# Kernel tuning notes

Hardware: AMD Instinct MI355X
Metric: run time of the kernel (lower is better)

## Reference

```python
import jax, jax.numpy as jnp
import numpy as np

N_NODES = 50000
N_EDGES = 640000
IN_CH, HID_CH, OUT_CH = 128, 128, 64


def setup_inputs() -> dict:
    key = jax.random.key(0)
    k1, k2, k3, k4, k5, k6 = jax.random.split(key, 6)
    x = jax.random.normal(k1, (N_NODES, IN_CH), dtype=jnp.float32)
    edge_index = jax.random.randint(k2, (2, N_EDGES), 0, N_NODES, dtype=jnp.int64)
    # Glorot-style init for GCN weights, zero bias (PyG defaults)
    W1 = jax.random.normal(k3, (IN_CH, HID_CH), dtype=jnp.float32) * (1.0 / np.sqrt(IN_CH))
    b1 = jnp.zeros((HID_CH,), dtype=jnp.float32)
    W2 = jax.random.normal(k4, (HID_CH, OUT_CH), dtype=jnp.float32) * (1.0 / np.sqrt(HID_CH))
    b2 = jnp.zeros((OUT_CH,), dtype=jnp.float32)
    return {"x": x, "edge_index": edge_index, "W1": W1, "b1": b1, "W2": W2, "b2": b2}


def gcn_conv(x, edge_index, W, b):
    """PyG GCNConv: add self-loops, symmetric deg^-1/2 normalization, linear, scatter-add."""
    N = x.shape[0]
    h = x @ W  # [N, C_out]
    loop = jnp.arange(N, dtype=edge_index.dtype)
    row = jnp.concatenate([edge_index[0], loop])  # source nodes
    col = jnp.concatenate([edge_index[1], loop])  # destination nodes
    deg = jax.ops.segment_sum(jnp.ones_like(col, dtype=h.dtype), col, num_segments=N)
    deg_inv_sqrt = jnp.where(deg > 0, deg ** -0.5, 0.0)
    norm = deg_inv_sqrt[row] * deg_inv_sqrt[col]  # [E+N]
    msg = h[row] * norm[:, None]  # gather + scale
    out = jax.ops.segment_sum(msg, col, num_segments=N)  # scatter-add
    return out + b


def reference(x, edge_index, W1, b1, W2, b2):
    h = jax.nn.relu(gcn_conv(x, edge_index, W1, b1))
    return gcn_conv(h, edge_index, W2, b2)
```

## Files before the change

### kernel.cpp

```cpp
#include <hip/hip_runtime.h>

#define NN 50000
#define NE 640000
#define NBK 196
#define CHUNK 2560

typedef __attribute__((ext_vector_type(8))) short s8v;
typedef __attribute__((ext_vector_type(4))) float f4v;

__device__ __forceinline__ unsigned short f2bf(float x) {
  unsigned int u = __float_as_uint(x);
  return (unsigned short)((u + 0x7fffu + ((u >> 16) & 1u)) >> 16);
}
__device__ __forceinline__ float bfval(unsigned short h) {
  return __uint_as_float((unsigned int)h << 16);
}
__device__ __forceinline__ float2 bfpair(unsigned int u) {
  float2 r;
  r.x = __uint_as_float((u & 0xffffu) << 16);
  r.y = __uint_as_float(u & 0xffff0000u);
  return r;
}

__device__ __forceinline__ void gload_lds16(const void* g, void* l) {
  __builtin_amdgcn_global_load_lds(
      (const __attribute__((address_space(1))) void*)g,
      (__attribute__((address_space(3))) void*)l, 16, 0, 0);
}


__global__ __launch_bounds__(256) void wprep_kernel(
    const float* __restrict__ W1, const float* __restrict__ W2,
    unsigned short* __restrict__ wt1h, unsigned short* __restrict__ wt1l,
    unsigned short* __restrict__ wt2h, unsigned short* __restrict__ wt2l,
    int* __restrict__ bcnt, unsigned int* __restrict__ htz, unsigned int* __restrict__ z1z) {
  const int b = blockIdx.x;
  const int t = threadIdx.x;
  if (b == 96) {
    for (int i = t; i < 2 * NBK; i += 256) bcnt[i] = 0;
    if (t < 64) htz[t] = 0u;
    if (t < 64) z1z[t] = 0u;
    return;
  }
  int idx = b * 256 + t;
  if (idx < 16384) {
    int c = idx >> 7, k = idx & 127;
    float w = W1[k * 128 + c];
    unsigned short h = f2bf(w);
    wt1h[idx] = h;
    wt1l[idx] = f2bf(w - bfval(h));
  } else if (idx < 24576) {
    int i2 = idx - 16384;
    int c = i2 >> 7, k = i2 & 127;
    float w = W2[k * 64 + c];
    unsigned short h = f2bf(w);
    wt2h[i2] = h;
    wt2l[i2] = f2bf(w - bfval(h));
  }
}


__global__ __launch_bounds__(256) void bucket_count_kernel(const int* __restrict__ col,
                                                           int* __restrict__ bcnt) {
  __shared__ int h[NBK];
  const int tid = threadIdx.x;
  for (int i = tid; i < NBK; i += 256) h[i] = 0;
  __syncthreads();
  const int base = blockIdx.x * CHUNK;
  for (int i = tid; i < CHUNK; i += 256) atomicAdd(&h[col[base + i] >> 8], 1);
  __syncthreads();
  for (int i = tid; i < NBK; i += 256)
    if (h[i]) atomicAdd(&bcnt[i], h[i]);
}

__global__ __launch_bounds__(256) void bucket_scatter_kernel(
    const int* __restrict__ row, const int* __restrict__ col,
    const int* __restrict__ bcnt, int* __restrict__ bfill,
    unsigned int* __restrict__ ebuf) {
  __shared__ int h[NBK], gst[NBK], h2[NBK], boffl[NBK], sc[256];
  const int tid = threadIdx.x;
  for (int i = tid; i < NBK; i += 256) { h[i] = 0; h2[i] = 0; }
  int v = (tid < NBK) ? bcnt[tid] : 0;
  sc[tid] = v;
  __syncthreads();
  for (int off = 1; off < 256; off <<= 1) {
    int u = (tid >= off) ? sc[tid - off] : 0;
    __syncthreads();
    sc[tid] += u;
    __syncthreads();
  }
  if (tid < NBK) boffl[tid] = sc[tid] - v;
  __syncthreads();

  const int base = blockIdx.x * CHUNK;
  for (int i = tid; i < CHUNK; i += 256) atomicAdd(&h[col[base + i] >> 8], 1);
  __syncthreads();
  for (int i = tid; i < NBK; i += 256) gst[i] = h[i] ? atomicAdd(&bfill[i], h[i]) : 0;
  __syncthreads();
  for (int i = tid; i < CHUNK; i += 256) {
    int c = col[base + i];
    int b = c >> 8;
    int r = atomicAdd(&h2[b], 1);
    unsigned int packed = ((unsigned int)row[base + i] << 8) | (unsigned int)(c & 255);
    ebuf[boffl[b] + gst[b] + r] = packed;
  }
}

__global__ __launch_bounds__(256) void bucket_build_kernel(
    const unsigned int* __restrict__ ebuf, const int* __restrict__ bcnt,
    int* __restrict__ row_ptr, float* __restrict__ dis, int* __restrict__ csr, int n) {
  __shared__ int cnt[256], c2[256], lbase[256], wsum[4], sc[256], cb[256];
  const int tid = threadIdx.x;
  const int b = blockIdx.x;

  int v = (tid < NBK) ? bcnt[tid] : 0;
  sc[tid] = v;
  cb[tid] = v;
  cnt[tid] = 0;
  c2[tid] = 0;
  __syncthreads();
  for (int off = 1; off < 256; off <<= 1) {
    int u = (tid >= off) ? sc[tid - off] : 0;
    __syncthreads();
    sc[tid] += u;
    __syncthreads();
  }
  const int s1 = sc[b];
  const int s0 = s1 - cb[b];

  for (int i = s0 + tid; i < s1; i += 256) atomicAdd(&cnt[ebuf[i] & 255], 1);
  __syncthreads();

  const int lane = tid & 63, w = tid >> 6;
  int c = cnt[tid];
  int inc = c;
#pragma unroll
  for (int off = 1; off < 64; off <<= 1) {
    int u = __shfl_up(inc, off);
    if (lane >= off) inc += u;
  }
  if (lane == 63) wsum[w] = inc;
  __syncthreads();
  int wo = 0;
  for (int i = 0; i < w; ++i) wo += wsum[i];
  const int excl = wo + inc - c;

  const int node = b * 256 + tid;
  if (node <= n) row_ptr[node] = s0 + excl;
  if (node < n) dis[node] = rsqrtf((float)(c + 1));
  lbase[tid] = s0 + excl;
  __syncthreads();

  for (int i = s0 + tid; i < s1; i += 256) {
    unsigned int p = ebuf[i];
    int dl = p & 255;
    int r = atomicAdd(&c2[dl], 1);
    csr[lbase[dl] + r] = (int)(p >> 8);
  }
}


template <int BM, int NCOLS, bool AF32, bool OUTBF16>
__global__ __launch_bounds__(256) void gemm_mfma_kernel(
    const void* __restrict__ Av, const unsigned short* __restrict__ Bth,
    const unsigned short* __restrict__ Btl, const float* __restrict__ dis,
    void* __restrict__ outv, int M) {
  constexpr int WCOL = NCOLS / 64;
  constexpr int WROW = 4 / WCOL;
  constexpr int RG = BM / (WROW * 16);
  constexpr int A_BYTES = BM * 32 * (AF32 ? 4 : 2);
  constexpr int B_BYTES = NCOLS * 32 * 2;
  constexpr int TILE_BYTES = A_BYTES + 2 * B_BYTES;
  constexpr int STAGE_BYTES = 2 * TILE_BYTES;
  constexpr int EPI_PITCH = OUTBF16 ? (NCOLS + 8) : (NCOLS + 4);
  constexpr int EPI_BYTES = BM * EPI_PITCH * (OUTBF16 ? 2 : 4);
  constexpr int SMEM_BYTES = STAGE_BYTES > EPI_BYTES ? STAGE_BYTES : EPI_BYTES;

  __shared__ __align__(16) unsigned char smem[SMEM_BYTES];

  const int t = threadIdx.x;
  const int lane = t & 63;
  const int l15 = lane & 15;
  const int lg = lane >> 4;
  const int wv = t >> 6;
  const int wr = wv % WROW;
  const int wc = wv / WROW;
  const int rb = blockIdx.x * BM;

  auto stage = [&](int kt, int buf) {
    unsigned char* base = smem + buf * TILE_BYTES;
    if constexpr (AF32) {
      constexpr int CPW = (BM * 128 / 1024) / 4;
#pragma unroll
      for (int j = 0; j < CPW; ++j) {
        int callr = (wv * CPW + j) * 8;
        int gr = min(rb + callr + (lane >> 3), M - 1);
        const float* gp = (const float*)Av + (size_t)gr * 128 + kt * 32 + (lane & 7) * 4;
        gload_lds16(gp, base + callr * 128);
      }
    } else {
      constexpr int CPW = (BM * 64 / 1024) / 4;
#pragma unroll
      for (int j = 0; j < CPW; ++j) {
        int callr = (wv * CPW + j) * 16;
        int gr = min(rb + callr + (lane >> 2), M - 1);
        const unsigned short* gp =
            (const unsigned short*)Av + (size_t)gr * 128 + kt * 32 + (lane & 3) * 8;
        gload_lds16(gp, base + callr * 64);
      }
    }
    {
      constexpr int CPW = (NCOLS * 64 / 1024) / 4;
#pragma unroll
      for (int j = 0; j < CPW; ++j) {
        int callr = (wv * CPW + j) * 16;
        int r = callr + (lane >> 2);
        size_t goff = (size_t)r * 128 + kt * 32 + (lane & 3) * 8;
        gload_lds16(Bth + goff, base + A_BYTES + callr * 64);
        gload_lds16(Btl + goff, base + A_BYTES + B_BYTES + callr * 64);
      }
    }
  };

  f4v acc[RG][4];
#pragma unroll
  for (int i = 0; i < RG; ++i)
#pragma unroll
    for (int j = 0; j < 4; ++j) acc[i][j] = (f4v){0.f, 0.f, 0.f, 0.f};

  stage(0, 0);
  __syncthreads();

#pragma unroll
  for (int kt = 0; kt < 4; ++kt) {
    const int buf = kt & 1;
    if (kt < 3) stage(kt + 1, buf ^ 1);

    const unsigned char* tb = smem + buf * TILE_BYTES;
    s8v afh[RG], afl[RG];
#pragma unroll
    for (int rg = 0; rg < RG; ++rg) {
      int row = wr * (RG * 16) + rg * 16 + l15;
      if constexpr (AF32) {
        const float* ap = (const float*)tb + row * 32 + lg * 8;
        float4 x0 = *reinterpret_cast<const float4*>(ap);
        float4 x1 = *reinterpret_cast<const float4*>(ap + 4);
        float f[8] = {x0.x, x0.y, x0.z, x0.w, x1.x, x1.y, x1.z, x1.w};
#pragma unroll
        for (int q = 0; q < 8; ++q) {
          unsigned short hq = f2bf(f[q]);
          afh[rg][q] = (short)hq;
          afl[rg][q] = (short)f2bf(f[q] - bfval(hq));
        }
      } else {
        afh[rg] = *reinterpret_cast<const s8v*>((const unsigned short*)tb + row * 32 + lg * 8);
      }
    }
#pragma unroll
    for (int cg = 0; cg < 4; ++cg) {
      int colr = wc * 64 + cg * 16 + l15;
      s8v bh = *reinterpret_cast<const s8v*>(
          (const unsigned short*)(tb + A_BYTES) + colr * 32 + lg * 8);
      s8v bl = *reinterpret_cast<const s8v*>(
          (const unsigned short*)(tb + A_BYTES + B_BYTES) + colr * 32 + lg * 8);
#pragma unroll
      for (int rg = 0; rg < RG; ++rg) {
        acc[rg][cg] = __builtin_amdgcn_mfma_f32_16x16x32_bf16(afh[rg], bh, acc[rg][cg], 0, 0, 0);
        acc[rg][cg] = __builtin_amdgcn_mfma_f32_16x16x32_bf16(afh[rg], bl, acc[rg][cg], 0, 0, 0);
        if constexpr (AF32)
          acc[rg][cg] = __builtin_amdgcn_mfma_f32_16x16x32_bf16(afl[rg], bh, acc[rg][cg], 0, 0, 0);
      }
    }
    __syncthreads();
  }

  float dv[RG][4];
#pragma unroll
  for (int rg = 0; rg < RG; ++rg)
#pragma unroll
    for (int g = 0; g < 4; ++g) {
      int r = rb + wr * (RG * 16) + rg * 16 + lg * 4 + g;
      dv[rg][g] = (r < M) ? dis[r] : 0.f;
    }

#pragma unroll
  for (int rg = 0; rg < RG; ++rg)
#pragma unroll
    for (int cg = 0; cg < 4; ++cg) {
      int colc = wc * 64 + cg * 16 + l15;
#pragma unroll
      for (int g = 0; g < 4; ++g) {
        int r = wr * (RG * 16) + rg * 16 + lg * 4 + g;
        float o = acc[rg][cg][g] * dv[rg][g];
        if constexpr (OUTBF16)
          ((unsigned short*)smem)[r * EPI_PITCH + colc] = f2bf(o);
        else
          ((float*)smem)[r * EPI_PITCH + colc] = o;
      }
    }
  __syncthreads();

  constexpr int CHR = OUTBF16 ? (NCOLS / 8) : (NCOLS / 4);
#pragma unroll
  for (int itc = 0; itc < BM * CHR / 256; ++itc) {
    int ch = t + itc * 256;
    int r = ch / CHR, cc = ch % CHR;
    if (rb + r < M) {
      if constexpr (OUTBF16) {
        int4 v = *reinterpret_cast<const int4*>(&((unsigned short*)smem)[r * EPI_PITCH + cc * 8]);
        *reinterpret_cast<int4*>(&((unsigned short*)outv)[(size_t)(rb + r) * NCOLS + cc * 8]) = v;
      } else {
        int4 v = *reinterpret_cast<const int4*>(&((float*)smem)[r * EPI_PITCH + cc * 4]);
        *reinterpret_cast<int4*>(&((float*)outv)[(size_t)(rb + r) * NCOLS + cc * 4]) = v;
      }
    }
  }
}


__global__ __launch_bounds__(256) void agg_bf16_kernel(
    const uint2* __restrict__ H2, const int* __restrict__ row_ptr,
    const int* __restrict__ csr, const float* __restrict__ dis,
    const float* __restrict__ bias, uint2* __restrict__ Z2, int n) {
  const int lane = threadIdx.x & 63;
  const int sub = lane & 31;
  int node = blockIdx.x * 8 + ((threadIdx.x >> 6) << 1) + (lane >> 5);
  if (node >= n) node = n - 1;

  const int s0 = row_ptr[node], s1 = row_ptr[node + 1];
  const int m = s1 - s0;
  const int mo = __shfl(m, lane ^ 32);
  const int mmax = m > mo ? m : mo;

  float4 a[8];
  {
    uint2 v = H2[node * 32 + sub];
    float2 p0 = bfpair(v.x), p1 = bfpair(v.y);
    a[0] = make_float4(p0.x, p0.y, p1.x, p1.y);
  }
#pragma unroll
  for (int i = 1; i < 8; ++i) a[i] = make_float4(0.f, 0.f, 0.f, 0.f);

  for (int e = 0; e < mmax; e += 32) {
    int idx = n;
    if (sub < m - e) idx = csr[s0 + e + sub];
    int jm = mmax - e;
    if (jm > 32) jm = 32;
    int j = 0;
    for (; j + 8 <= jm; j += 8) {
      int r0 = __shfl(idx, j, 32),     r1 = __shfl(idx, j + 1, 32);
      int r2 = __shfl(idx, j + 2, 32), r3 = __shfl(idx, j + 3, 32);
      int r4 = __shfl(idx, j + 4, 32), r5 = __shfl(idx, j + 5, 32);
      int r6 = __shfl(idx, j + 6, 32), r7 = __shfl(idx, j + 7, 32);
      uint2 v0 = H2[r0 * 32 + sub], v1 = H2[r1 * 32 + sub];
      uint2 v2 = H2[r2 * 32 + sub], v3 = H2[r3 * 32 + sub];
      uint2 v4 = H2[r4 * 32 + sub], v5 = H2[r5 * 32 + sub];
      uint2 v6 = H2[r6 * 32 + sub], v7 = H2[r7 * 32 + sub];
      float2 p;
      p = bfpair(v0.x); a[0].x += p.x; a[0].y += p.y; p = bfpair(v0.y); a[0].z += p.x; a[0].w += p.y;
      p = bfpair(v1.x); a[1].x += p.x; a[1].y += p.y; p = bfpair(v1.y); a[1].z += p.x; a[1].w += p.y;
      p = bfpair(v2.x); a[2].x += p.x; a[2].y += p.y; p = bfpair(v2.y); a[2].z += p.x; a[2].w += p.y;
      p = bfpair(v3.x); a[3].x += p.x; a[3].y += p.y; p = bfpair(v3.y); a[3].z += p.x; a[3].w += p.y;
      p = bfpair(v4.x); a[4].x += p.x; a[4].y += p.y; p = bfpair(v4.y); a[4].z += p.x; a[4].w += p.y;
      p = bfpair(v5.x); a[5].x += p.x; a[5].y += p.y; p = bfpair(v5.y); a[5].z += p.x; a[5].w += p.y;
      p = bfpair(v6.x); a[6].x += p.x; a[6].y += p.y; p = bfpair(v6.y); a[6].z += p.x; a[6].w += p.y;
      p = bfpair(v7.x); a[7].x += p.x; a[7].y += p.y; p = bfpair(v7.y); a[7].z += p.x; a[7].w += p.y;
    }
    for (; j + 4 <= jm; j += 4) {
      int r0 = __shfl(idx, j, 32),     r1 = __shfl(idx, j + 1, 32);
      int r2 = __shfl(idx, j + 2, 32), r3 = __shfl(idx, j + 3, 32);
      uint2 v0 = H2[r0 * 32 + sub], v1 = H2[r1 * 32 + sub];
      uint2 v2 = H2[r2 * 32 + sub], v3 = H2[r3 * 32 + sub];
      float2 p;
      p = bfpair(v0.x); a[0].x += p.x; a[0].y += p.y; p = bfpair(v0.y); a[0].z += p.x; a[0].w += p.y;
      p = bfpair(v1.x); a[1].x += p.x; a[1].y += p.y; p = bfpair(v1.y); a[1].z += p.x; a[1].w += p.y;
      p = bfpair(v2.x); a[2].x += p.x; a[2].y += p.y; p = bfpair(v2.y); a[2].z += p.x; a[2].w += p.y;
      p = bfpair(v3.x); a[3].x += p.x; a[3].y += p.y; p = bfpair(v3.y); a[3].z += p.x; a[3].w += p.y;
    }
    for (; j < jm; ++j) {
      int r0 = __shfl(idx, j, 32);
      uint2 v0 = H2[r0 * 32 + sub];
      float2 p;
      p = bfpair(v0.x); a[0].x += p.x; a[0].y += p.y; p = bfpair(v0.y); a[0].z += p.x; a[0].w += p.y;
    }
  }
  float4 s;
  s.x = ((a[0].x + a[1].x) + (a[2].x + a[3].x)) + ((a[4].x + a[5].x) + (a[6].x + a[7].x));
  s.y = ((a[0].y + a[1].y) + (a[2].y + a[3].y)) + ((a[4].y + a[5].y) + (a[6].y + a[7].y));
  s.z = ((a[0].z + a[1].z) + (a[2].z + a[3].z)) + ((a[4].z + a[5].z) + (a[6].z + a[7].z));
  s.w = ((a[0].w + a[1].w) + (a[2].w + a[3].w)) + ((a[4].w + a[5].w) + (a[6].w + a[7].w));
  const float d = dis[node];
  float4 b = reinterpret_cast<const float4*>(bias)[sub];
  float ox = fmaxf(s.x * d + b.x, 0.f);
  float oy = fmaxf(s.y * d + b.y, 0.f);
  float oz = fmaxf(s.z * d + b.z, 0.f);
  float ow = fmaxf(s.w * d + b.w, 0.f);
  uint2 o;
  o.x = (unsigned int)f2bf(ox) | ((unsigned int)f2bf(oy) << 16);
  o.y = (unsigned int)f2bf(oz) | ((unsigned int)f2bf(ow) << 16);
  Z2[node * 32 + sub] = o;
}

__global__ __launch_bounds__(256) void agg_f32_kernel(
    const float2* __restrict__ Hs2, const int* __restrict__ row_ptr,
    const int* __restrict__ csr, const float* __restrict__ dis,
    const float* __restrict__ bias, float2* __restrict__ out2, int n) {
  const int lane = threadIdx.x & 63;
  const int sub = lane & 31;
  int node = blockIdx.x * 8 + ((threadIdx.x >> 6) << 1) + (lane >> 5);
  if (node >= n) node = n - 1;

  const int s0 = row_ptr[node], s1 = row_ptr[node + 1];
  const int m = s1 - s0;
  const int mo = __shfl(m, lane ^ 32);
  const int mmax = m > mo ? m : mo;

  float2 a[8];
  a[0] = Hs2[node * 32 + sub];
#pragma unroll
  for (int i = 1; i < 8; ++i) a[i] = make_float2(0.f, 0.f);

  for (int e = 0; e < mmax; e += 32) {
    int idx = n;
    if (sub < m - e) idx = csr[s0 + e + sub];
    int jm = mmax - e;
    if (jm > 32) jm = 32;
    int j = 0;
    for (; j + 8 <= jm; j += 8) {
      int r0 = __shfl(idx, j, 32),     r1 = __shfl(idx, j + 1, 32);
      int r2 = __shfl(idx, j + 2, 32), r3 = __shfl(idx, j + 3, 32);
      int r4 = __shfl(idx, j + 4, 32), r5 = __shfl(idx, j + 5, 32);
      int r6 = __shfl(idx, j + 6, 32), r7 = __shfl(idx, j + 7, 32);
      float2 v0 = Hs2[r0 * 32 + sub], v1 = Hs2[r1 * 32 + sub];
      float2 v2 = Hs2[r2 * 32 + sub], v3 = Hs2[r3 * 32 + sub];
      float2 v4 = Hs2[r4 * 32 + sub], v5 = Hs2[r5 * 32 + sub];
      float2 v6 = Hs2[r6 * 32 + sub], v7 = Hs2[r7 * 32 + sub];
      a[0].x += v0.x; a[0].y += v0.y;  a[1].x += v1.x; a[1].y += v1.y;
      a[2].x += v2.x; a[2].y += v2.y;  a[3].x += v3.x; a[3].y += v3.y;
      a[4].x += v4.x; a[4].y += v4.y;  a[5].x += v5.x; a[5].y += v5.y;
      a[6].x += v6.x; a[6].y += v6.y;  a[7].x += v7.x; a[7].y += v7.y;
    }
    for (; j + 4 <= jm; j += 4) {
      int r0 = __shfl(idx, j, 32),     r1 = __shfl(idx, j + 1, 32);
      int r2 = __shfl(idx, j + 2, 32), r3 = __shfl(idx, j + 3, 32);
      float2 v0 = Hs2[r0 * 32 + sub], v1 = Hs2[r1 * 32 + sub];
      float2 v2 = Hs2[r2 * 32 + sub], v3 = Hs2[r3 * 32 + sub];
      a[0].x += v0.x; a[0].y += v0.y;  a[1].x += v1.x; a[1].y += v1.y;
      a[2].x += v2.x; a[2].y += v2.y;  a[3].x += v3.x; a[3].y += v3.y;
    }
    for (; j < jm; ++j) {
      float2 v = Hs2[__shfl(idx, j, 32) * 32 + sub];
      a[0].x += v.x; a[0].y += v.y;
    }
  }
  float sx = ((a[0].x + a[1].x) + (a[2].x + a[3].x)) + ((a[4].x + a[5].x) + (a[6].x + a[7].x));
  float sy = ((a[0].y + a[1].y) + (a[2].y + a[3].y)) + ((a[4].y + a[5].y) + (a[6].y + a[7].y));
  const float d = dis[node];
  float2 b = reinterpret_cast<const float2*>(bias)[sub];
  out2[node * 32 + sub] = make_float2(sx * d + b.x, sy * d + b.y);
}


extern "C" void kernel_launch(void* const* d_in, const int* in_sizes, int n_in,
                              void* d_out, int out_size, void* d_ws, size_t ws_size,
                              hipStream_t stream) {
  const float* x  = (const float*)d_in[0];
  const int*   ei = (const int*)d_in[1];
  const float* W1 = (const float*)d_in[2];
  const float* b1 = (const float*)d_in[3];
  const float* W2 = (const float*)d_in[4];
  const float* b2 = (const float*)d_in[5];
  float* out = (float*)d_out;

  const int* row = ei;
  const int* col = ei + NE;

  char* ws = (char*)d_ws;
  size_t off = 0;
  auto alloc = [&](size_t bytes) -> void* {
    off = (off + 255) & ~(size_t)255;
    void* p = ws + off;
    off += bytes;
    return p;
  };

  int* bcnt    = (int*)alloc((size_t)2 * NBK * sizeof(int));
  int* bfill   = bcnt + NBK;
  unsigned int* ebuf = (unsigned int*)alloc((size_t)NE * sizeof(unsigned int));
  int* row_ptr = (int*)alloc((size_t)(NN + 1) * sizeof(int));
  int* csr     = (int*)alloc((size_t)NE * sizeof(int));
  float* dis   = (float*)alloc((size_t)NN * sizeof(float));
  unsigned short* wt1h = (unsigned short*)alloc((size_t)(2 * 128 * 128 + 2 * 64 * 128) * 2);
  unsigned short* wt1l = wt1h + 128 * 128;
  unsigned short* wt2h = wt1l + 128 * 128;
  unsigned short* wt2l = wt2h + 64 * 128;
  unsigned short* HT16 = (unsigned short*)alloc((size_t)(NN + 1) * 128 * 2);
  float* HT32 = (float*)HT16;
  unsigned short* Z1 = (unsigned short*)alloc((size_t)(NN + 1) * 128 * 2);

  wprep_kernel<<<97, 256, 0, stream>>>(W1, W2, wt1h, wt1l, wt2h, wt2l, bcnt,
                                       (unsigned int*)(HT16 + (size_t)NN * 128),
                                       (unsigned int*)(Z1 + (size_t)NN * 128));
  bucket_count_kernel<<<NE / CHUNK, 256, 0, stream>>>(col, bcnt);
  bucket_scatter_kernel<<<NE / CHUNK, 256, 0, stream>>>(row, col, bcnt, bfill, ebuf);
  bucket_build_kernel<<<NBK, 256, 0, stream>>>(ebuf, bcnt, row_ptr, dis, csr, NN);

  const int ga = (NN + 7) / 8;

  gemm_mfma_kernel<64, 128, true, true><<<(NN + 63) / 64, 256, 0, stream>>>(
      x, wt1h, wt1l, dis, HT16, NN);
  agg_bf16_kernel<<<ga, 256, 0, stream>>>((const uint2*)HT16, row_ptr, csr, dis, b1,
                                          (uint2*)Z1, NN);

  gemm_mfma_kernel<64, 64, false, false><<<(NN + 63) / 64, 256, 0, stream>>>(
      Z1, wt2h, wt2l, dis, HT32, NN);
  agg_f32_kernel<<<ga, 256, 0, stream>>>((const float2*)HT32, row_ptr, csr, dis, b2,
                                         (float2*)out, NN);
}
```

Before: 120.0 us.

## Compute degrees via global atomics and fuse CSR build with first GEMM launch

Node degrees are now counted with global atomics in the count pass, and the inverse square roots are produced inside the scatter kernel. That removes the dependency of the first GEMM on the CSR build, so the bucket build blocks and the first GEMM blocks run in one launch and overlap. This cuts one kernel launch and idle tail time. The cost is 640k extra global atomics and an extra zeroing pass over the count array.

After: 132.9 us. +10.7%, slower.

```diff
diff --git a/kernel.cpp b/kernel.cpp
--- a/kernel.cpp
+++ b/kernel.cpp
@@ -4,6 +4,7 @@
 #define NE 640000
 #define NBK 196
 #define CHUNK 2560
+#define NCB 250
 
 typedef __attribute__((ext_vector_type(8))) short s8v;
 typedef __attribute__((ext_vector_type(4))) float f4v;
@@ -17,7 +18,7 @@
 }
 __device__ __forceinline__ float2 bfpair(unsigned int u) {
   float2 r;
-  r.x = __uint_as_float((u & 0xffffu) << 16);
+  r.x = __uint_as_float(u << 16);
   r.y = __uint_as_float(u & 0xffff0000u);
   return r;
 }
@@ -29,56 +30,72 @@
 }
 
 
-__global__ __launch_bounds__(256) void wprep_kernel(
+__global__ __launch_bounds__(256) void init_kernel(
     const float* __restrict__ W1, const float* __restrict__ W2,
     unsigned short* __restrict__ wt1h, unsigned short* __restrict__ wt1l,
     unsigned short* __restrict__ wt2h, unsigned short* __restrict__ wt2l,
-    int* __restrict__ bcnt, unsigned int* __restrict__ htz, unsigned int* __restrict__ z1z) {
+    int* __restrict__ bcnt, unsigned int* __restrict__ htz,
+    unsigned int* __restrict__ z1z, int* __restrict__ cnt) {
   const int b = blockIdx.x;
   const int t = threadIdx.x;
-  if (b == 96) {
+  if (b < 96) {
+    int idx = b * 256 + t;
+    if (idx < 16384) {
+      int c = idx >> 7, k = idx & 127;
+      float w = W1[k * 128 + c];
+      unsigned short h = f2bf(w);
+      wt1h[idx] = h;
+      wt1l[idx] = f2bf(w - bfval(h));
+    } else {
+      int i2 = idx - 16384;
+      int c = i2 >> 7, k = i2 & 127;
+      float w = W2[k * 64 + c];
+      unsigned short h = f2bf(w);
+      wt2h[i2] = h;
+      wt2l[i2] = f2bf(w - bfval(h));
+    }
+  } else if (b == 96) {
     for (int i = t; i < 2 * NBK; i += 256) bcnt[i] = 0;
     if (t < 64) htz[t] = 0u;
     if (t < 64) z1z[t] = 0u;
-    return;
-  }
-  int idx = b * 256 + t;
-  if (idx < 16384) {
-    int c = idx >> 7, k = idx & 127;
-    float w = W1[k * 128 + c];
-    unsigned short h = f2bf(w);
-    wt1h[idx] = h;
-    wt1l[idx] = f2bf(w - bfval(h));
-  } else if (idx < 24576) {
-    int i2 = idx - 16384;
-    int c = i2 >> 7, k = i2 & 127;
-    float w = W2[k * 64 + c];
-    unsigned short h = f2bf(w);
-    wt2h[i2] = h;
-    wt2l[i2] = f2bf(w - bfval(h));
-  }
-}
-
-
-__global__ __launch_bounds__(256) void bucket_count_kernel(const int* __restrict__ col,
-                                                           int* __restrict__ bcnt) {
+  } else {
+    int base = (b - 97) * 1024;
+    for (int i = base + t; i < base + 1024 && i < NN; i += 256) cnt[i] = 0;
+  }
+}
+
+
+__global__ __launch_bounds__(256) void count_kernel(const int* __restrict__ col,
+                                                    int* __restrict__ cnt,
+                                                    int* __restrict__ bcnt) {
   __shared__ int h[NBK];
   const int tid = threadIdx.x;
   for (int i = tid; i < NBK; i += 256) h[i] = 0;
   __syncthreads();
   const int base = blockIdx.x * CHUNK;
-  for (int i = tid; i < CHUNK; i += 256) atomicAdd(&h[col[base + i] >> 8], 1);
+  for (int i = tid; i < CHUNK; i += 256) {
+    int c = col[base + i];
+    atomicAdd(&cnt[c], 1);
+    atomicAdd(&h[c >> 8], 1);
+  }
   __syncthreads();
   for (int i = tid; i < NBK; i += 256)
     if (h[i]) atomicAdd(&bcnt[i], h[i]);
 }
 
-__global__ __launch_bounds__(256) void bucket_scatter_kernel(
+
+__global__ __launch_bounds__(256) void scatter_dis_kernel(
     const int* __restrict__ row, const int* __restrict__ col,
     const int* __restrict__ bcnt, int* __restrict__ bfill,
-    unsigned int* __restrict__ ebuf) {
+    unsigned int* __restrict__ ebuf, const int* __restrict__ cnt,
+    float* __restrict__ dis) {
+  const int tid = threadIdx.x;
+  if (blockIdx.x >= NCB) {
+    int node = (blockIdx.x - NCB) * 256 + tid;
+    if (node < NN) dis[node] = rsqrtf((float)(cnt[node] + 1));
+    return;
+  }
   __shared__ int h[NBK], gst[NBK], h2[NBK], boffl[NBK], sc[256];
-  const int tid = threadIdx.x;
   for (int i = tid; i < NBK; i += 256) { h[i] = 0; h2[i] = 0; }
   int v = (tid < NBK) ? bcnt[tid] : 0;
   sc[tid] = v;
@@ -106,89 +123,38 @@
   }
 }
 
-__global__ __launch_bounds__(256) void bucket_build_kernel(
-    const unsigned int* __restrict__ ebuf, const int* __restrict__ bcnt,
-    int* __restrict__ row_ptr, float* __restrict__ dis, int* __restrict__ csr, int n) {
-  __shared__ int cnt[256], c2[256], lbase[256], wsum[4], sc[256], cb[256];
-  const int tid = threadIdx.x;
-  const int b = blockIdx.x;
-
-  int v = (tid < NBK) ? bcnt[tid] : 0;
-  sc[tid] = v;
-  cb[tid] = v;
-  cnt[tid] = 0;
-  c2[tid] = 0;
-  __syncthreads();
-  for (int off = 1; off < 256; off <<= 1) {
-    int u = (tid >= off) ? sc[tid - off] : 0;
-    __syncthreads();
-    sc[tid] += u;
-    __syncthreads();
-  }
-  const int s1 = sc[b];
-  const int s0 = s1 - cb[b];
-
-  for (int i = s0 + tid; i < s1; i += 256) atomicAdd(&cnt[ebuf[i] & 255], 1);
-  __syncthreads();
-
-  const int lane = tid & 63, w = tid >> 6;
-  int c = cnt[tid];
-  int inc = c;
-#pragma unroll
-  for (int off = 1; off < 64; off <<= 1) {
-    int u = __shfl_up(inc, off);
-    if (lane >= off) inc += u;
-  }
-  if (lane == 63) wsum[w] = inc;
-  __syncthreads();
-  int wo = 0;
-  for (int i = 0; i < w; ++i) wo += wsum[i];
-  const int excl = wo + inc - c;
-
-  const int node = b * 256 + tid;
-  if (node <= n) row_ptr[node] = s0 + excl;
-  if (node < n) dis[node] = rsqrtf((float)(c + 1));
-  lbase[tid] = s0 + excl;
-  __syncthreads();
-
-  for (int i = s0 + tid; i < s1; i += 256) {
-    unsigned int p = ebuf[i];
-    int dl = p & 255;
-    int r = atomicAdd(&c2[dl], 1);
-    csr[lbase[dl] + r] = (int)(p >> 8);
-  }
-}
-
 
 template <int BM, int NCOLS, bool AF32, bool OUTBF16>
-__global__ __launch_bounds__(256) void gemm_mfma_kernel(
-    const void* __restrict__ Av, const unsigned short* __restrict__ Bth,
-    const unsigned short* __restrict__ Btl, const float* __restrict__ dis,
-    void* __restrict__ outv, int M) {
-  constexpr int WCOL = NCOLS / 64;
-  constexpr int WROW = 4 / WCOL;
-  constexpr int RG = BM / (WROW * 16);
-  constexpr int A_BYTES = BM * 32 * (AF32 ? 4 : 2);
-  constexpr int B_BYTES = NCOLS * 32 * 2;
-  constexpr int TILE_BYTES = A_BYTES + 2 * B_BYTES;
-  constexpr int STAGE_BYTES = 2 * TILE_BYTES;
-  constexpr int EPI_PITCH = OUTBF16 ? (NCOLS + 8) : (NCOLS + 4);
-  constexpr int EPI_BYTES = BM * EPI_PITCH * (OUTBF16 ? 2 : 4);
-  constexpr int SMEM_BYTES = STAGE_BYTES > EPI_BYTES ? STAGE_BYTES : EPI_BYTES;
-
-  __shared__ __align__(16) unsigned char smem[SMEM_BYTES];
-
+struct GemmCfg {
+  static constexpr int WCOL = NCOLS / 64;
+  static constexpr int WROW = 4 / WCOL;
+  static constexpr int RG = BM / (WROW * 16);
+  static constexpr int A_BYTES = BM * 32 * (AF32 ? 4 : 2);
+  static constexpr int B_BYTES = NCOLS * 32 * 2;
+  static constexpr int TILE_BYTES = A_BYTES + 2 * B_BYTES;
+  static constexpr int STAGE_BYTES = 2 * TILE_BYTES;
+  static constexpr int EPI_PITCH = OUTBF16 ? (NCOLS + 8) : (NCOLS + 4);
+  static constexpr int EPI_BYTES = BM * EPI_PITCH * (OUTBF16 ? 2 : 4);
+  static constexpr int SMEM = STAGE_BYTES > EPI_BYTES ? STAGE_BYTES : EPI_BYTES;
+};
+
+template <int BM, int NCOLS, bool AF32, bool OUTBF16>
+__device__ __forceinline__ void gemm_body(
+    unsigned char* smem, int bid, const void* __restrict__ Av,
+    const unsigned short* __restrict__ Bth, const unsigned short* __restrict__ Btl,
+    const float* __restrict__ dis, void* __restrict__ outv, int M) {
+  using C = GemmCfg<BM, NCOLS, AF32, OUTBF16>;
   const int t = threadIdx.x;
   const int lane = t & 63;
   const int l15 = lane & 15;
   const int lg = lane >> 4;
   const int wv = t >> 6;
-  const int wr = wv % WROW;
-  const int wc = wv / WROW;
-  const int rb = blockIdx.x * BM;
+  const int wr = wv % C::WROW;
+  const int wc = wv / C::WROW;
+  const int rb = bid * BM;
 
   auto stage = [&](int kt, int buf) {
-    unsigned char* base = smem + buf * TILE_BYTES;
+    unsigned char* base = smem + buf * C::TILE_BYTES;
     if constexpr (AF32) {
       constexpr int CPW = (BM * 128 / 1024) / 4;
 #pragma unroll
@@ -216,15 +182,15 @@
         int callr = (wv * CPW + j) * 16;
         int r = callr + (lane >> 2);
         size_t goff = (size_t)r * 128 + kt * 32 + (lane & 3) * 8;
-        gload_lds16(Bth + goff, base + A_BYTES + callr * 64);
-        gload_lds16(Btl + goff, base + A_BYTES + B_BYTES + callr * 64);
+        gload_lds16(Bth + goff, base + C::A_BYTES + callr * 64);
+        gload_lds16(Btl + goff, base + C::A_BYTES + C::B_BYTES + callr * 64);
       }
     }
   };
 
-  f4v acc[RG][4];
-#pragma unroll
-  for (int i = 0; i < RG; ++i)
+  f4v acc[C::RG][4];
+#pragma unroll
+  for (int i = 0; i < C::RG; ++i)
 #pragma unroll
     for (int j = 0; j < 4; ++j) acc[i][j] = (f4v){0.f, 0.f, 0.f, 0.f};
 
@@ -236,13 +202,13 @@
     const int buf = kt & 1;
     if (kt < 3) stage(kt + 1, buf ^ 1);
 
-    const unsigned char* tb = smem + buf * TILE_BYTES;
-    s8v afh[RG], afl[RG];
-#pragma unroll
-    for (int rg = 0; rg < RG; ++rg) {
-      int row = wr * (RG * 16) + rg * 16 + l15;
+    const unsigned char* tb = smem + buf * C::TILE_BYTES;
+    s8v afh[C::RG], afl[C::RG];
+#pragma unroll
+    for (int rg = 0; rg < C::RG; ++rg) {
+      int rrow = wr * (C::RG * 16) + rg * 16 + l15;
       if constexpr (AF32) {
-        const float* ap = (const float*)tb + row * 32 + lg * 8;
+        const float* ap = (const float*)tb + rrow * 32 + lg * 8;
         float4 x0 = *reinterpret_cast<const float4*>(ap);
         float4 x1 = *reinterpret_cast<const float4*>(ap + 4);
         float f[8] = {x0.x, x0.y, x0.z, x0.w, x1.x, x1.y, x1.z, x1.w};
@@ -253,18 +219,18 @@
           afl[rg][q] = (short)f2bf(f[q] - bfval(hq));
         }
       } else {
-        afh[rg] = *reinterpret_cast<const s8v*>((const unsigned short*)tb + row * 32 + lg * 8);
+        afh[rg] = *reinterpret_cast<const s8v*>((const unsigned short*)tb + rrow * 32 + lg * 8);
       }
     }
 #pragma unroll
     for (int cg = 0; cg < 4; ++cg) {
       int colr = wc * 64 + cg * 16 + l15;
       s8v bh = *reinterpret_cast<const s8v*>(
-          (const unsigned short*)(tb + A_BYTES) + colr * 32 + lg * 8);
+          (const unsigned short*)(tb + C::A_BYTES) + colr * 32 + lg * 8);
       s8v bl = *reinterpret_cast<const s8v*>(
-          (const unsigned short*)(tb + A_BYTES + B_BYTES) + colr * 32 + lg * 8);
-#pragma unroll
-      for (int rg = 0; rg < RG; ++rg) {
+          (const unsigned short*)(tb + C::A_BYTES + C::B_BYTES) + colr * 32 + lg * 8);
+#pragma unroll
+      for (int rg = 0; rg < C::RG; ++rg) {
         acc[rg][cg] = __builtin_amdgcn_mfma_f32_16x16x32_bf16(afh[rg], bh, acc[rg][cg], 0, 0, 0);
         acc[rg][cg] = __builtin_amdgcn_mfma_f32_16x16x32_bf16(afh[rg], bl, acc[rg][cg], 0, 0, 0);
         if constexpr (AF32)
@@ -274,28 +240,28 @@
     __syncthreads();
   }
 
-  float dv[RG][4];
-#pragma unroll
-  for (int rg = 0; rg < RG; ++rg)
+  float dv[C::RG][4];
+#pragma unroll
+  for (int rg = 0; rg < C::RG; ++rg)
 #pragma unroll
     for (int g = 0; g < 4; ++g) {
-      int r = rb + wr * (RG * 16) + rg * 16 + lg * 4 + g;
+      int r = rb + wr * (C::RG * 16) + rg * 16 + lg * 4 + g;
       dv[rg][g] = (r < M) ? dis[r] : 0.f;
     }
 
 #pragma unroll
-  for (int rg = 0; rg < RG; ++rg)
+  for (int rg = 0; rg < C::RG; ++rg)
 #pragma unroll
     for (int cg = 0; cg < 4; ++cg) {
       int colc = wc * 64 + cg * 16 + l15;
 #pragma unroll
       for (int g = 0; g < 4; ++g) {
-        int r = wr * (RG * 16) + rg * 16 + lg * 4 + g;
+        int r = wr * (C::RG * 16) + rg * 16 + lg * 4 + g;
         float o = acc[rg][cg][g] * dv[rg][g];
         if constexpr (OUTBF16)
-          ((unsigned short*)smem)[r * EPI_PITCH + colc] = f2bf(o);
+          ((unsigned short*)smem)[r * C::EPI_PITCH + colc] = f2bf(o);
         else
-          ((float*)smem)[r * EPI_PITCH + colc] = o;
+          ((float*)smem)[r * C::EPI_PITCH + colc] = o;
       }
     }
   __syncthreads();
@@ -307,14 +273,94 @@
     int r = ch / CHR, cc = ch % CHR;
     if (rb + r < M) {
       if constexpr (OUTBF16) {
-        int4 v = *reinterpret_cast<const int4*>(&((unsigned short*)smem)[r * EPI_PITCH + cc * 8]);
+        int4 v = *reinterpret_cast<const int4*>(&((unsigned short*)smem)[r * C::EPI_PITCH + cc * 8]);
         *reinterpret_cast<int4*>(&((unsigned short*)outv)[(size_t)(rb + r) * NCOLS + cc * 8]) = v;
       } else {
-        int4 v = *reinterpret_cast<const int4*>(&((float*)smem)[r * EPI_PITCH + cc * 4]);
+        int4 v = *reinterpret_cast<const int4*>(&((float*)smem)[r * C::EPI_PITCH + cc * 4]);
         *reinterpret_cast<int4*>(&((float*)outv)[(size_t)(rb + r) * NCOLS + cc * 4]) = v;
       }
     }
   }
+}
+
+
+__global__ __launch_bounds__(256) void build_gemm1_kernel(
+    const unsigned int* __restrict__ ebuf, const int* __restrict__ bcnt,
+    int* __restrict__ row_ptr, int* __restrict__ csr,
+    const float* __restrict__ x, const unsigned short* __restrict__ wt1h,
+    const unsigned short* __restrict__ wt1l, const float* __restrict__ dis,
+    void* __restrict__ HT16, int n) {
+  using C = GemmCfg<64, 128, true, true>;
+  __shared__ __align__(16) unsigned char smem[C::SMEM];
+
+  if (blockIdx.x >= NBK) {
+    gemm_body<64, 128, true, true>(smem, blockIdx.x - NBK, x, wt1h, wt1l, dis, HT16, n);
+    return;
+  }
+
+  int* cnt_  = (int*)smem;
+  int* c2    = cnt_ + 256;
+  int* lbase = c2 + 256;
+  int* sc    = lbase + 256;
+  int* cb    = sc + 256;
+  int* wsum  = cb + 256;
+
+  const int tid = threadIdx.x;
+  const int b = blockIdx.x;
+
+  int v = (tid < NBK) ? bcnt[tid] : 0;
+  sc[tid] = v;
+  cb[tid] = v;
+  cnt_[tid] = 0;
+  c2[tid] = 0;
+  __syncthreads();
+  for (int off = 1; off < 256; off <<= 1) {
+    int u = (tid >= off) ? sc[tid - off] : 0;
+    __syncthreads();
+    sc[tid] += u;
+    __syncthreads();
+  }
+  const int s1 = sc[b];
+  const int s0 = s1 - cb[b];
+
+  for (int i = s0 + tid; i < s1; i += 256) atomicAdd(&cnt_[ebuf[i] & 255], 1);
+  __syncthreads();
+
+  const int lane = tid & 63, w = tid >> 6;
+  int c = cnt_[tid];
+  int inc = c;
+#pragma unroll
+  for (int off = 1; off < 64; off <<= 1) {
+    int u = __shfl_up(inc, off);
+    if (lane >= off) inc += u;
+  }
+  if (lane == 63) wsum[w] = inc;
+  __syncthreads();
+  int wo = 0;
+  for (int i = 0; i < w; ++i) wo += wsum[i];
+  const int excl = wo + inc - c;
+
+  const int node = b * 256 + tid;
+  if (node <= n) row_ptr[node] = s0 + excl;
+  lbase[tid] = s0 + excl;
+  __syncthreads();
+
+  for (int i = s0 + tid; i < s1; i += 256) {
+    unsigned int p = ebuf[i];
+    int dl = p & 255;
+    int r = atomicAdd(&c2[dl], 1);
+    csr[lbase[dl] + r] = (int)(p >> 8);
+  }
+}
+
+
+__global__ __launch_bounds__(256) void gemm2_kernel(
+    const void* __restrict__ Z1, const unsigned short* __restrict__ wt2h,
+    const unsigned short* __restrict__ wt2l, const float* __restrict__ dis,
+    void* __restrict__ HT32, int n) {
+  using C = GemmCfg<64, 64, false, false>;
+  __shared__ __align__(16) unsigned char smem[C::SMEM];
+  gemm_body<64, 64, false, false>(smem, blockIdx.x, Z1, wt2h, wt2l, dis, HT32, n);
 }
 
 
@@ -378,8 +424,7 @@
       p = bfpair(v3.x); a[3].x += p.x; a[3].y += p.y; p = bfpair(v3.y); a[3].z += p.x; a[3].w += p.y;
     }
     for (; j < jm; ++j) {
-      int r0 = __shfl(idx, j, 32);
-      uint2 v0 = H2[r0 * 32 + sub];
+      uint2 v0 = H2[__shfl(idx, j, 32) * 32 + sub];
       float2 p;
       p = bfpair(v0.x); a[0].x += p.x; a[0].y += p.y; p = bfpair(v0.y); a[0].z += p.x; a[0].w += p.y;
     }
@@ -486,6 +531,7 @@
 
   int* bcnt    = (int*)alloc((size_t)2 * NBK * sizeof(int));
   int* bfill   = bcnt + NBK;
+  int* cnt     = (int*)alloc((size_t)NN * sizeof(int));
   unsigned int* ebuf = (unsigned int*)alloc((size_t)NE * sizeof(unsigned int));
   int* row_ptr = (int*)alloc((size_t)(NN + 1) * sizeof(int));
   int* csr     = (int*)alloc((size_t)NE * sizeof(int));
@@ -498,22 +544,18 @@
   float* HT32 = (float*)HT16;
   unsigned short* Z1 = (unsigned short*)alloc((size_t)(NN + 1) * 128 * 2);
 
-  wprep_kernel<<<97, 256, 0, stream>>>(W1, W2, wt1h, wt1l, wt2h, wt2l, bcnt,
+  init_kernel<<<146, 256, 0, stream>>>(W1, W2, wt1h, wt1l, wt2h, wt2l, bcnt,
                                        (unsigned int*)(HT16 + (size_t)NN * 128),
-                                       (unsigned int*)(Z1 + (size_t)NN * 128));
-  bucket_count_kernel<<<NE / CHUNK, 256, 0, stream>>>(col, bcnt);
-  bucket_scatter_kernel<<<NE / CHUNK, 256, 0, stream>>>(row, col, bcnt, bfill, ebuf);
-  bucket_build_kernel<<<NBK, 256, 0, stream>>>(ebuf, bcnt, row_ptr, dis, csr, NN);
+                                       (unsigned int*)(Z1 + (size_t)NN * 128), cnt);
+  count_kernel<<<NCB, 256, 0, stream>>>(col, cnt, bcnt);
+  scatter_dis_kernel<<<NCB + 196, 256, 0, stream>>>(row, col, bcnt, bfill, ebuf, cnt, dis);
+  build_gemm1_kernel<<<NBK + (NN + 63) / 64, 256, 0, stream>>>(
+      ebuf, bcnt, row_ptr, csr, x, wt1h, wt1l, dis, HT16, NN);
 
   const int ga = (NN + 7) / 8;
-
-  gemm_mfma_kernel<64, 128, true, true><<<(NN + 63) / 64, 256, 0, stream>>>(
-      x, wt1h, wt1l, dis, HT16, NN);
   agg_bf16_kernel<<<ga, 256, 0, stream>>>((const uint2*)HT16, row_ptr, csr, dis, b1,
                                           (uint2*)Z1, NN);
-
-  gemm_mfma_kernel<64, 64, false, false><<<(NN + 63) / 64, 256, 0, stream>>>(
-      Z1, wt2h, wt2l, dis, HT32, NN);
+  gemm2_kernel<<<(NN + 63) / 64, 256, 0, stream>>>(Z1, wt2h, wt2l, dis, HT32, NN);
   agg_f32_kernel<<<ga, 256, 0, stream>>>((const float2*)HT32, row_ptr, csr, dis, b2,
                                          (float2*)out, NN);
 }
```
